# Performance work log

Hardware: AMD Instinct MI355X
Metric: run time of the kernel (lower is better)

## Reference

```python
import jax, jax.numpy as jnp
import numpy as np

BN_EPS = 1e-5


def setup_inputs() -> dict:
    key = jax.random.key(0)
    ks = jax.random.split(key, 5)
    num = 65536
    x = jax.random.normal(ks[0], (num, 3, 256), dtype=jnp.float32)
    w1a = jax.random.normal(ks[1], (256, 768), dtype=jnp.float32) * (1.0 / np.sqrt(256))
    w2a = jax.random.normal(ks[2], (256, 768), dtype=jnp.float32) * (1.0 / np.sqrt(256))
    w1b = jax.random.normal(ks[3], (768, 768), dtype=jnp.float32) * (1.0 / np.sqrt(768))
    w2b = jax.random.normal(ks[4], (768, 768), dtype=jnp.float32) * (1.0 / np.sqrt(768))
    gamma = jnp.ones((768,), dtype=jnp.float32)
    beta = jnp.zeros((768,), dtype=jnp.float32)
    return {"x": x, "w1a": w1a, "w2a": w2a, "w1b": w1b, "w2b": w2b,
            "gamma": gamma, "beta": beta, "num": num}


def _sage_layer(h, w1, w2):
    # h: [num, 3, d_in]. For each hop, neighbors = mean of the other 2 hops
    # = (sum_over_hops - self) / 2. Then self @ w2 + neigh @ w1 (no activation,
    # matching the source which defines ReLU but never applies it).
    neigh = (h.sum(axis=1, keepdims=True) - h) * 0.5          # [num, 3, d_in]
    return jnp.einsum('nhd,de->nhe', h, w2) + jnp.einsum('nhd,de->nhe', neigh, w1)


def reference(x, w1a, w2a, w1b, w2b, gamma, beta, num):
    h = _sage_layer(x, w1a, w2a)      # [num, 3, 768]
    h = _sage_layer(h, w1b, w2b)      # [num, 3, 768]
    out = h[:, 0, :]                  # take hop 0 per graph item -> [num, 768]
    # BatchNorm1d(768), training mode: biased batch stats over the num axis
    mean = out.mean(axis=0)
    var = out.var(axis=0)             # ddof=0, matches torch normalization
    out = (out - mean) * jax.lax.rsqrt(var + BN_EPS) * gamma + beta
    return jax.nn.sigmoid(out)
```

## Files before the change

kernel.cpp:

```cpp
#include <hip/hip_runtime.h>
#include <cstdint>
#include <cstddef>

#define NSAMP 65536
#define KDIM  512
#define MDIM  768

typedef __attribute__((ext_vector_type(8))) _Float16 f16x8;
typedef __attribute__((ext_vector_type(4))) float f32x4;

union H2U { _Float16 h; unsigned short u; };
__device__ __forceinline__ unsigned short f2h(float f) {
  H2U v; v.h = (_Float16)f; return v.u;
}
__device__ __forceinline__ float h2f(unsigned short u) {
  H2U v; v.u = u; return (float)v.h;
}

__global__ __launch_bounds__(256) void prep_A_kernel(const float* __restrict__ x,
                                                     unsigned short* __restrict__ A) {
  int gid = blockIdx.x * 256 + threadIdx.x;
  int n  = gid >> 6;
  int cg = gid & 63;
  const float4* xr = (const float4*)(x + (size_t)n * 768);
  float4 a = xr[cg];
  float4 b = xr[64 + cg];
  float4 c = xr[128 + cg];
  ushort4 lo, hi;
  lo.x = f2h(a.x); lo.y = f2h(a.y); lo.z = f2h(a.z); lo.w = f2h(a.w);
  hi.x = f2h(a.x + b.x + c.x); hi.y = f2h(a.y + b.y + c.y);
  hi.z = f2h(a.z + b.z + c.z); hi.w = f2h(a.w + b.w + c.w);
  unsigned short* Arow = A + (size_t)n * KDIM;
  *(ushort4*)(Arow + cg * 4) = lo;
  *(ushort4*)(Arow + 256 + cg * 4) = hi;
}

__global__ __launch_bounds__(256) void prep_B_partial(const float* __restrict__ w1a,
                                                      const float* __restrict__ w2a,
                                                      const float* __restrict__ w1b,
                                                      const float* __restrict__ w2b,
                                                      float* __restrict__ temp) {
  int b = blockIdx.x;
  int jc = b & 3;
  int rem = b >> 2;
  int mc = rem % 3;
  int ic = rem / 3;
  int t = threadIdx.x;
  int m = mc * 256 + t;
  int i0 = ic * 8;
  int j0 = jc * 192;
  __shared__ __align__(16) float sC[8][192];
  __shared__ __align__(16) float s1[8][192];
  __shared__ __align__(16) float s2[8][192];
  for (int idx = t; idx < 8 * 192; idx += 256) {
    int ii = idx / 192, jj = idx % 192;
    float a1 = w1a[(size_t)(i0 + ii) * 768 + j0 + jj];
    float a2 = w2a[(size_t)(i0 + ii) * 768 + j0 + jj];
    s1[ii][jj] = a1; s2[ii][jj] = a2; sC[ii][jj] = a2 - 0.5f * a1;
  }
  __syncthreads();
  float acc1[8] = {0,0,0,0,0,0,0,0};
  float acc2[8] = {0,0,0,0,0,0,0,0};
  const float* pb1 = w1b + (size_t)j0 * 768 + m;
  const float* pb2 = w2b + (size_t)j0 * 768 + m;
  for (int jb = 0; jb < 192; jb += 4) {
    float F[4], Gp[4], Hh[4];
#pragma unroll
    for (int u = 0; u < 4; ++u) {
      float b1 = pb1[(size_t)(jb + u) * 768];
      float b2 = pb2[(size_t)(jb + u) * 768];
      F[u]  = b2 - 0.5f * b1;
      Gp[u] = 0.5f * b2 + 0.25f * b1;
      Hh[u] = 0.5f * b1;
    }
#pragma unroll
    for (int ii = 0; ii < 8; ++ii) {
      f32x4 c  = *(const f32x4*)&sC[ii][jb];
      f32x4 a1 = *(const f32x4*)&s1[ii][jb];
      f32x4 a2 = *(const f32x4*)&s2[ii][jb];
#pragma unroll
      for (int u = 0; u < 4; ++u) {
        acc1[ii] += c[u] * F[u];
        acc2[ii] += a1[u] * Gp[u] + a2[u] * Hh[u];
      }
    }
  }
  float* t1 = temp + ((size_t)jc * 768 + m) * 256 + i0;
  float* t2 = temp + ((size_t)(4 + jc) * 768 + m) * 256 + i0;
#pragma unroll
  for (int ii = 0; ii < 8; ++ii) { t1[ii] = acc1[ii]; t2[ii] = acc2[ii]; }
}

__global__ __launch_bounds__(256) void prep_B_convert(const float* __restrict__ temp,
                                                      unsigned short* __restrict__ Bt,
                                                      float* __restrict__ stats) {
  int idx = blockIdx.x * 256 + threadIdx.x;
  int i = idx & 255;
  int m = idx >> 8;
  const float* t1 = temp + (size_t)m * 256 + i;
  const float* t2 = temp + ((size_t)4 * 768 + m) * 256 + i;
  float v1 = 0.f, v2 = 0.f;
#pragma unroll
  for (int jc = 0; jc < 4; ++jc) {
    v1 += t1[(size_t)jc * 768 * 256];
    v2 += t2[(size_t)jc * 768 * 256];
  }
  Bt[(size_t)m * KDIM + i]       = f2h(v1);
  Bt[(size_t)m * KDIM + 256 + i] = f2h(v2);
  if (idx < 1536) stats[idx] = 0.f;
}

template <bool F16OUT>
__global__ __launch_bounds__(256) void gemm_kernel(const unsigned short* __restrict__ A,
                                                   const unsigned short* __restrict__ Bt,
                                                   float* __restrict__ outf,
                                                   unsigned short* __restrict__ outh,
                                                   float* __restrict__ stats) {
  int bid = blockIdx.x;
  int swz = (bid & 7) * 384 + (bid >> 3);
  int bm  = swz % 6;
  int bn  = swz / 6;
  int tid  = threadIdx.x;
  int wid  = tid >> 6;
  int lane = tid & 63;
  int quad = lane >> 4;
  int l15  = lane & 15;
  int wave_r = wid >> 1;
  int wave_c = wid & 1;

  size_t row0 = (size_t)bn * 128;
  int    col0 = bm * 128;

  f32x4 acc[4][4];
#pragma unroll
  for (int i = 0; i < 4; ++i)
#pragma unroll
    for (int j = 0; j < 4; ++j) acc[i][j] = (f32x4)(0.f);

  const unsigned short* baseA = A  + (row0 + wave_r * 64 + l15) * KDIM + quad * 8;
  const unsigned short* baseB = Bt + (size_t)(col0 + wave_c * 64 + l15) * KDIM + quad * 8;

#define LOADSET(aF, bF, kk)                                                        \
  do {                                                                             \
    _Pragma("unroll")                                                              \
    for (int rb = 0; rb < 4; ++rb)                                                 \
      aF[rb] = *(const f16x8*)(baseA + (size_t)rb * (16 * KDIM) + (kk));           \
    _Pragma("unroll")                                                              \
    for (int cb = 0; cb < 4; ++cb)                                                 \
      bF[cb] = *(const f16x8*)(baseB + (size_t)cb * (16 * KDIM) + (kk));           \
  } while (0)

#define MFMASET(aF, bF)                                                            \
  do {                                                                             \
    _Pragma("unroll")                                                              \
    for (int rb = 0; rb < 4; ++rb)                                                 \
      _Pragma("unroll")                                                            \
      for (int cb = 0; cb < 4; ++cb)                                               \
        acc[rb][cb] =                                                              \
            __builtin_amdgcn_mfma_f32_16x16x32_f16(aF[rb], bF[cb], acc[rb][cb],    \
                                                   0, 0, 0);                       \
  } while (0)

  f16x8 a0[4], b0[4], a1[4], b1[4];
  LOADSET(a0, b0, 0);
#pragma unroll
  for (int k0 = 0; k0 < KDIM; k0 += 64) {
    LOADSET(a1, b1, k0 + 32);
    MFMASET(a0, b0);
    if (k0 + 64 < KDIM) LOADSET(a0, b0, k0 + 64);
    MFMASET(a1, b1);
  }
#undef LOADSET
#undef MFMASET

#pragma unroll
  for (int cb = 0; cb < 4; ++cb) {
    int col = col0 + wave_c * 64 + cb * 16 + l15;
    float s1 = 0.f, s2 = 0.f;
#pragma unroll
    for (int rb = 0; rb < 4; ++rb) {
      size_t rg = row0 + wave_r * 64 + rb * 16 + quad * 4;
#pragma unroll
      for (int reg = 0; reg < 4; ++reg) {
        float v = acc[rb][cb][reg];
        if (F16OUT) outh[(rg + reg) * MDIM + col] = f2h(v);
        else        outf[(rg + reg) * MDIM + col] = v;
        s1 += v;
        s2 += v * v;
      }
    }
    s1 += __shfl_xor(s1, 16); s1 += __shfl_xor(s1, 32);
    s2 += __shfl_xor(s2, 16); s2 += __shfl_xor(s2, 32);
    if (quad == 0) {
      atomicAdd(&stats[col], s1);
      atomicAdd(&stats[768 + col], s2);
    }
  }
}

__global__ void finalize_stats(const float* __restrict__ stats, const float* __restrict__ gamma,
                               const float* __restrict__ beta, float* __restrict__ ss) {
  int c = threadIdx.x;
  if (c < 768) {
    const float inv_n = 1.0f / 65536.0f;
    float mean = stats[c] * inv_n;
    float ex2  = stats[768 + c] * inv_n;
    float var  = ex2 - mean * mean;
    float scale = gamma[c] * rsqrtf(var + 1e-5f);
    ss[c]       = scale;
    ss[768 + c] = beta[c] - mean * scale;
  }
}

__global__ __launch_bounds__(256) void bn_sigmoid_h(const unsigned short* __restrict__ outpre,
                                                    const float* __restrict__ ss,
                                                    float* __restrict__ out) {
  int idx = blockIdx.x * 256 + threadIdx.x;
  int cg  = (idx % 96) * 8;
  f16x8 h = *(const f16x8*)(outpre + (size_t)idx * 8);
  float4 sc0 = *(const float4*)&ss[cg];
  float4 sc1 = *(const float4*)&ss[cg + 4];
  float4 sh0 = *(const float4*)&ss[768 + cg];
  float4 sh1 = *(const float4*)&ss[768 + cg + 4];
  float4 r0, r1;
  r0.x = 1.f / (1.f + __expf(-((float)h[0] * sc0.x + sh0.x)));
  r0.y = 1.f / (1.f + __expf(-((float)h[1] * sc0.y + sh0.y)));
  r0.z = 1.f / (1.f + __expf(-((float)h[2] * sc0.z + sh0.z)));
  r0.w = 1.f / (1.f + __expf(-((float)h[3] * sc0.w + sh0.w)));
  r1.x = 1.f / (1.f + __expf(-((float)h[4] * sc1.x + sh1.x)));
  r1.y = 1.f / (1.f + __expf(-((float)h[5] * sc1.y + sh1.y)));
  r1.z = 1.f / (1.f + __expf(-((float)h[6] * sc1.z + sh1.z)));
  r1.w = 1.f / (1.f + __expf(-((float)h[7] * sc1.w + sh1.w)));
  ((float4*)out)[(size_t)idx * 2]     = r0;
  ((float4*)out)[(size_t)idx * 2 + 1] = r1;
}

__global__ __launch_bounds__(256) void bn_sigmoid_f(float* __restrict__ out,
                                                    const float* __restrict__ ss) {
  int idx = blockIdx.x * 256 + threadIdx.x;
  int cg  = (idx % 192) * 4;
  float4 v  = ((const float4*)out)[idx];
  float4 sc = *(const float4*)&ss[cg];
  float4 sh = *(const float4*)&ss[768 + cg];
  v.x = 1.f / (1.f + __expf(-(v.x * sc.x + sh.x)));
  v.y = 1.f / (1.f + __expf(-(v.y * sc.y + sh.y)));
  v.z = 1.f / (1.f + __expf(-(v.z * sc.z + sh.z)));
  v.w = 1.f / (1.f + __expf(-(v.w * sc.w + sh.w)));
  ((float4*)out)[idx] = v;
}

extern "C" void kernel_launch(void* const* d_in, const int* in_sizes, int n_in,
                              void* d_out, int out_size, void* d_ws, size_t ws_size,
                              hipStream_t stream) {
  const float* x     = (const float*)d_in[0];
  const float* w1a   = (const float*)d_in[1];
  const float* w2a   = (const float*)d_in[2];
  const float* w1b   = (const float*)d_in[3];
  const float* w2b   = (const float*)d_in[4];
  const float* gamma = (const float*)d_in[5];
  const float* beta  = (const float*)d_in[6];
  float* out = (float*)d_out;

  size_t offA     = 0;
  size_t offBt    = offA + (size_t)NSAMP * KDIM * 2;
  size_t offTemp  = offBt + (size_t)MDIM * KDIM * 2;
  size_t offStats = offTemp + (size_t)2 * 4 * 768 * 256 * 4;
  size_t offSS    = offStats + 1536 * 4;
  size_t offOut   = (offSS + 1536 * 4 + 255) & ~(size_t)255;
  size_t needF16  = offOut + (size_t)NSAMP * MDIM * 2;

  unsigned short* A    = (unsigned short*)((char*)d_ws + offA);
  unsigned short* Bt   = (unsigned short*)((char*)d_ws + offBt);
  float* temp          = (float*)((char*)d_ws + offTemp);
  float* stats         = (float*)((char*)d_ws + offStats);
  float* ss            = (float*)((char*)d_ws + offSS);
  unsigned short* oh   = (unsigned short*)((char*)d_ws + offOut);
  bool f16stage = ws_size >= needF16;

  prep_A_kernel<<<NSAMP * 64 / 256, 256, 0, stream>>>(x, A);
  prep_B_partial<<<384, 256, 0, stream>>>(w1a, w2a, w1b, w2b, temp);
  prep_B_convert<<<768, 256, 0, stream>>>(temp, Bt, stats);
  if (f16stage) {
    gemm_kernel<true><<<(NSAMP / 128) * (MDIM / 128), 256, 0, stream>>>(A, Bt, nullptr, oh, stats);
    finalize_stats<<<1, 768, 0, stream>>>(stats, gamma, beta, ss);
    bn_sigmoid_h<<<(size_t)NSAMP * MDIM / 8 / 256, 256, 0, stream>>>(oh, ss, out);
  } else {
    gemm_kernel<false><<<(NSAMP / 128) * (MDIM / 128), 256, 0, stream>>>(A, Bt, out, nullptr, stats);
    finalize_stats<<<1, 768, 0, stream>>>(stats, gamma, beta, ss);
    bn_sigmoid_f<<<(size_t)NSAMP * MDIM / 4 / 256, 256, 0, stream>>>(out, ss);
  }
}
```

Before: 662.5 us.

## Stage GEMM operand tiles through double-buffered LDS with direct global-to-LDS loads

Replaces per-wave direct global fragment loads in the GEMM with a double-buffered shared-memory pipeline. Tiles are filled using global_load_lds with an XOR swizzle to avoid bank conflicts. Each A/B element is fetched from global once per block instead of once per wave, and MFMA blocks are wrapped in s_setprio. The cost is extra barriers and hand-written vmcnt waits whose counts must match the issued loads.

```diff
diff --git a/kernel.cpp b/kernel.cpp
--- a/kernel.cpp
+++ b/kernel.cpp
@@ -116,6 +116,9 @@
                                                    float* __restrict__ outf,
                                                    unsigned short* __restrict__ outh,
                                                    float* __restrict__ stats) {
+  __shared__ __align__(16) unsigned short As[2 * 128 * 64];
+  __shared__ __align__(16) unsigned short Bs[2 * 128 * 64];
+
   int bid = blockIdx.x;
   int swz = (bid & 7) * 384 + (bid >> 3);
   int bm  = swz % 6;
@@ -137,41 +140,79 @@
 #pragma unroll
     for (int j = 0; j < 4; ++j) acc[i][j] = (f32x4)(0.f);
 
-  const unsigned short* baseA = A  + (row0 + wave_r * 64 + l15) * KDIM + quad * 8;
-  const unsigned short* baseB = Bt + (size_t)(col0 + wave_c * 64 + l15) * KDIM + quad * 8;
-
-#define LOADSET(aF, bF, kk)                                                        \
-  do {                                                                             \
-    _Pragma("unroll")                                                              \
-    for (int rb = 0; rb < 4; ++rb)                                                 \
-      aF[rb] = *(const f16x8*)(baseA + (size_t)rb * (16 * KDIM) + (kk));           \
-    _Pragma("unroll")                                                              \
-    for (int cb = 0; cb < 4; ++cb)                                                 \
-      bF[cb] = *(const f16x8*)(baseB + (size_t)cb * (16 * KDIM) + (kk));           \
+  int rsub = lane >> 3;
+  int ssw  = (lane & 7) ^ rsub;
+
+  const unsigned short* gA0 = A  + (row0 + wid * 8 + rsub) * KDIM + ssw * 8;
+  const unsigned short* gB0 = Bt + (size_t)(col0 + wid * 8 + rsub) * KDIM + ssw * 8;
+
+#define STAGE(buf, kk)                                                              \
+  do {                                                                              \
+    _Pragma("unroll")                                                               \
+    for (int i = 0; i < 4; ++i) {                                                   \
+      int rl = i * 32 + wid * 8;                                                    \
+      const unsigned short* gA = gA0 + (size_t)i * (32 * KDIM) + (kk);              \
+      const unsigned short* gB = gB0 + (size_t)i * (32 * KDIM) + (kk);              \
+      unsigned short* lA = As + (buf) * 8192 + rl * 64;                             \
+      unsigned short* lB = Bs + (buf) * 8192 + rl * 64;                             \
+      __builtin_amdgcn_global_load_lds(                                             \
+          (const __attribute__((address_space(1))) void*)(uintptr_t)gA,             \
+          (__attribute__((address_space(3))) void*)(uint32_t)(uintptr_t)lA, 16, 0, 0); \
+      __builtin_amdgcn_global_load_lds(                                             \
+          (const __attribute__((address_space(1))) void*)(uintptr_t)gB,             \
+          (__attribute__((address_space(3))) void*)(uint32_t)(uintptr_t)lB, 16, 0, 0); \
+    }                                                                               \
   } while (0)
 
-#define MFMASET(aF, bF)                                                            \
-  do {                                                                             \
-    _Pragma("unroll")                                                              \
-    for (int rb = 0; rb < 4; ++rb)                                                 \
-      _Pragma("unroll")                                                            \
-      for (int cb = 0; cb < 4; ++cb)                                               \
-        acc[rb][cb] =                                                              \
-            __builtin_amdgcn_mfma_f32_16x16x32_f16(aF[rb], bF[cb], acc[rb][cb],    \
-                                                   0, 0, 0);                       \
+#define COMPUTE(buf)                                                                \
+  do {                                                                              \
+    _Pragma("unroll")                                                               \
+    for (int ks = 0; ks < 2; ++ks) {                                                \
+      f16x8 a[4], b[4];                                                             \
+      _Pragma("unroll")                                                             \
+      for (int rb = 0; rb < 4; ++rb) {                                              \
+        int r  = wave_r * 64 + rb * 16 + l15;                                       \
+        int sl = (ks * 4 + quad) ^ (l15 & 7);                                       \
+        a[rb] = *(const f16x8*)&As[(buf) * 8192 + r * 64 + sl * 8];                 \
+      }                                                                             \
+      _Pragma("unroll")                                                             \
+      for (int cb = 0; cb < 4; ++cb) {                                              \
+        int r  = wave_c * 64 + cb * 16 + l15;                                       \
+        int sl = (ks * 4 + quad) ^ (l15 & 7);                                       \
+        b[cb] = *(const f16x8*)&Bs[(buf) * 8192 + r * 64 + sl * 8];                 \
+      }                                                                             \
+      __builtin_amdgcn_s_setprio(1);                                               \
+      _Pragma("unroll")                                                             \
+      for (int rb = 0; rb < 4; ++rb)                                                \
+        _Pragma("unroll")                                                           \
+        for (int cb = 0; cb < 4; ++cb)                                              \
+          acc[rb][cb] = __builtin_amdgcn_mfma_f32_16x16x32_f16(a[rb], b[cb],        \
+                                                               acc[rb][cb], 0, 0, 0); \
+      __builtin_amdgcn_s_setprio(0);                                               \
+    }                                                                               \
   } while (0)
 
-  f16x8 a0[4], b0[4], a1[4], b1[4];
-  LOADSET(a0, b0, 0);
-#pragma unroll
-  for (int k0 = 0; k0 < KDIM; k0 += 64) {
-    LOADSET(a1, b1, k0 + 32);
-    MFMASET(a0, b0);
-    if (k0 + 64 < KDIM) LOADSET(a0, b0, k0 + 64);
-    MFMASET(a1, b1);
-  }
-#undef LOADSET
-#undef MFMASET
+  STAGE(0, 0);
+#pragma unroll
+  for (int tt = 0; tt < 4; ++tt) {
+    const int k0 = tt * 128;
+    STAGE(1, k0 + 64);
+    asm volatile("s_waitcnt vmcnt(8)" ::: "memory");
+    __builtin_amdgcn_s_barrier();
+    COMPUTE(0);
+    __builtin_amdgcn_s_barrier();
+    if (tt < 3) {
+      STAGE(0, k0 + 128);
+      asm volatile("s_waitcnt vmcnt(8)" ::: "memory");
+    } else {
+      asm volatile("s_waitcnt vmcnt(0)" ::: "memory");
+    }
+    __builtin_amdgcn_s_barrier();
+    COMPUTE(1);
+    __builtin_amdgcn_s_barrier();
+  }
+#undef STAGE
+#undef COMPUTE
 
 #pragma unroll
   for (int cb = 0; cb < 4; ++cb) {
```

Measured after the change: 572.6 us. 1.16x faster.
